# Performance work log

Measured on AMD Instinct MI355X. Metric: run time of the kernel, lower is better.

Reference implementation:

```python
import jax, jax.numpy as jnp
import numpy as np

D = 768
H = 8
HD = D // H
MLP = 3072
EPS = 1e-5


def _ln(x, g, b):
    mu = jnp.mean(x, axis=-1, keepdims=True)
    var = jnp.var(x, axis=-1, keepdims=True)
    return (x - mu) * jax.lax.rsqrt(var + EPS) * g + b


def setup_inputs() -> dict:
    key = jax.random.key(0)
    ks = jax.random.split(key, 20)
    B, N = 4, 2048
    s = 0.02
    inp = {
        "x": jax.random.normal(ks[0], (B, N, D), jnp.float32),
        "position_bias": jax.random.normal(ks[1], (N, N), jnp.float32),
        "wq": jax.random.normal(ks[2], (D, D), jnp.float32) * s,
        "bq": jnp.zeros((D,), jnp.float32),
        "wk": jax.random.normal(ks[3], (D, D), jnp.float32) * s,
        "bk": jnp.zeros((D,), jnp.float32),
        "wv": jax.random.normal(ks[4], (D, D), jnp.float32) * s,
        "bv": jnp.zeros((D,), jnp.float32),
        "wo": jax.random.normal(ks[5], (D, D), jnp.float32) * s,
        "bo": jnp.zeros((D,), jnp.float32),
        "g1": jnp.ones((D,), jnp.float32),
        "b1": jnp.zeros((D,), jnp.float32),
        "g2": jnp.ones((D,), jnp.float32),
        "b2": jnp.zeros((D,), jnp.float32),
        "w_ff1": jax.random.normal(ks[6], (D, MLP), jnp.float32) * s,
        "b_ff1": jnp.zeros((MLP,), jnp.float32),
        "w_ff2": jax.random.normal(ks[7], (MLP, D), jnp.float32) * s,
        "b_ff2": jnp.zeros((D,), jnp.float32),
    }
    return inp


def reference(x, position_bias, wq, bq, wk, bk, wv, bv, wo, bo, g1, b1, g2, b2, w_ff1, b_ff1, w_ff2, b_ff2):
    B, N, _ = x.shape
    scale = HD ** -0.5
    # pre-norm attention
    n1 = _ln(x, g1, b1)
    q = (n1 @ wq + bq).reshape(B, N, H, HD).transpose(0, 2, 1, 3)
    k = (n1 @ wk + bk).reshape(B, N, H, HD).transpose(0, 2, 1, 3)
    v = (n1 @ wv + bv).reshape(B, N, H, HD).transpose(0, 2, 1, 3)
    attn = jnp.einsum('bhqd,bhkd->bhqk', q, k) * scale  # [B,H,N,N]
    attn = attn + position_bias[None, None, :, :]
    attn = jax.nn.softmax(attn, axis=-1)
    out = jnp.einsum('bhqk,bhkd->bhqd', attn, v)
    out = out.transpose(0, 2, 1, 3).reshape(B, N, D)
    out = out @ wo + bo
    x = x + out
    # pre-norm GELU MLP (exact erf gelu, torch default)
    n2 = _ln(x, g2, b2)
    h = jax.nn.gelu(n2 @ w_ff1 + b_ff1, approximate=False)
    x = x + (h @ w_ff2 + b_ff2)
    return x
```

## Files before the change

kernel.cpp:

```cpp
#include <hip/hip_runtime.h>
#include <hip/hip_bf16.h>

#define D 768
#define H 8
#define HD 96
#define MLP 3072
#define NB 2048
#define BATCH 4

typedef __attribute__((ext_vector_type(8))) short short8;
typedef __attribute__((ext_vector_type(4))) short short4v;
typedef __attribute__((ext_vector_type(4))) float f32x4;
typedef __attribute__((ext_vector_type(16))) float f32x16;
typedef __attribute__((ext_vector_type(4))) int int4v;

typedef const __attribute__((address_space(1))) unsigned int gu32;
typedef __attribute__((address_space(3))) unsigned int lu32;

__device__ inline void gload16(const void* g, void* l){
  __builtin_amdgcn_global_load_lds((gu32*)g, (lu32*)l, 16, 0, 0);
}

__device__ inline short f2b(float f){
  __hip_bfloat16 h = __float2bfloat16(f);
  return *reinterpret_cast<short*>(&h);
}
__device__ inline float b2f(short s){
  return __uint_as_float(((unsigned)(unsigned short)s) << 16);
}
__device__ inline float fexp2(float x){ return __builtin_amdgcn_exp2f(x); }

__device__ inline unsigned cvtpk(float lo, float hi){
  unsigned r;
  asm volatile("v_cvt_pk_bf16_f32 %0, %1, %2" : "=v"(r) : "v"(lo), "v"(hi));
  return r;
}

__global__ __launch_bounds__(256) void mega_prep(
    const float* __restrict__ x, const float* __restrict__ g1, const float* __restrict__ b1,
    short* __restrict__ n1,
    const float* __restrict__ wq, const float* __restrict__ wk, const float* __restrict__ wv,
    const float* __restrict__ wo, const float* __restrict__ wf1, const float* __restrict__ wf2,
    const float* __restrict__ bq, const float* __restrict__ bk, const float* __restrict__ bv,
    short* __restrict__ wqkv_t, short* __restrict__ wo_t,
    short* __restrict__ w1_t, short* __restrict__ w2_t, float* __restrict__ bqkv,
    const float* __restrict__ pb, short* __restrict__ pbT)
{
  __shared__ float shbuf[32*33];
  int bx = blockIdx.x;
  int t = threadIdx.x;
  if (bx < 8192){
    int row = bx;
    const float* xr = x + (size_t)row*D;
    float v0=xr[t], v1=xr[t+256], v2=xr[t+512];
    float s=v0+v1+v2, ss=v0*v0+v1*v1+v2*v2;
    #pragma unroll
    for (int m=1;m<64;m<<=1){ s += __shfl_xor(s,m); ss += __shfl_xor(ss,m); }
    int w=t>>6, lane=t&63;
    if (!lane){ shbuf[w]=s; shbuf[4+w]=ss; }
    __syncthreads();
    s = shbuf[0]+shbuf[1]+shbuf[2]+shbuf[3];
    ss = shbuf[4]+shbuf[5]+shbuf[6]+shbuf[7];
    float mu = s*(1.f/768.f);
    float inv = rsqrtf(ss*(1.f/768.f) - mu*mu + 1e-5f);
    short* o = n1 + (size_t)row*D;
    o[t]     = f2b((v0-mu)*inv*g1[t]     + b1[t]);
    o[t+256] = f2b((v1-mu)*inv*g1[t+256] + b1[t+256]);
    o[t+512] = f2b((v2-mu)*inv*g1[t+512] + b1[t+512]);
  } else if (bx < 15104){
    int i = bx - 8192;
    if (i < 3){
      int j = i*256 + t;
      bqkv[j] = bq[j]; bqkv[768+j] = bk[j]; bqkv[1536+j] = bv[j];
    }
    const float* in; short* out; int K, Nc, bk_, bn_;
    if (i < 2304){
      int which = i/576, ii = i - which*576;
      bk_ = ii%24; bn_ = ii/24; K = 768; Nc = 768;
      if      (which==0){ in = wq; out = wqkv_t; }
      else if (which==1){ in = wk; out = wqkv_t + 768*768; }
      else if (which==2){ in = wv; out = wqkv_t + 2*768*768; }
      else              { in = wo; out = wo_t; }
    } else if (i < 4608){
      int ii = i - 2304; bk_ = ii%24; bn_ = ii/24; K = 768; Nc = 3072; in = wf1; out = w1_t;
    } else {
      int ii = i - 4608; bk_ = ii%96; bn_ = ii/96; K = 3072; Nc = 768; in = wf2; out = w2_t;
    }
    float (*tile)[33] = (float(*)[33])shbuf;
    int tx = t & 31, ty = t >> 5;
    #pragma unroll
    for (int j=0;j<4;++j)
      tile[ty + j*8][tx] = in[(size_t)(bk_*32 + ty + j*8)*Nc + bn_*32 + tx];
    __syncthreads();
    #pragma unroll
    for (int j=0;j<4;++j)
      out[(size_t)(bn_*32 + ty + j*8)*K + bk_*32 + tx] = f2b(tile[tx][ty + j*8]);
  } else {
    int i = bx - 15104;
    int qt = i & 63, kb = i >> 6;
    int l = t >> 2;
    int vbase = (t & 3) * 8;
    int q = qt*32 + (l & 31);
    int hi = l >> 5;
    const float L2E = 1.4426950408889634f;
    short8 o;
    #pragma unroll
    for (int j=0;j<8;++j){
      int v = vbase + j;
      int r = v & 15, tile_ = v >> 4;
      int k = kb*64 + tile_*32 + 8*(r>>2) + (r&3) + 4*hi;
      o[j] = f2b(pb[(size_t)q*NB + k] * L2E);
    }
    *(short8*)&pbT[(((size_t)(qt*32 + kb))*64 + l)*32 + vbase] = o;
  }
}

__global__ __launch_bounds__(256) void ln_k(const float* __restrict__ X, const float* __restrict__ gg,
                                            const float* __restrict__ bb, short* __restrict__ out){
  int row = blockIdx.x, t = threadIdx.x;
  const float* x = X + (size_t)row*D;
  float v0=x[t], v1=x[t+256], v2=x[t+512];
  float s=v0+v1+v2, ss=v0*v0+v1*v1+v2*v2;
  #pragma unroll
  for (int m=1;m<64;m<<=1){ s += __shfl_xor(s,m); ss += __shfl_xor(ss,m); }
  __shared__ float red[8];
  int w=t>>6, lane=t&63;
  if (!lane){ red[w]=s; red[4+w]=ss; }
  __syncthreads();
  s = red[0]+red[1]+red[2]+red[3];
  ss = red[4]+red[5]+red[6]+red[7];
  float mu = s*(1.f/768.f);
  float inv = rsqrtf(ss*(1.f/768.f) - mu*mu + 1e-5f);
  short* o = out + (size_t)row*D;
  o[t]     = f2b((v0-mu)*inv*gg[t]     + bb[t]);
  o[t+256] = f2b((v1-mu)*inv*gg[t+256] + bb[t+256]);
  o[t+512] = f2b((v2-mu)*inv*gg[t+512] + bb[t+512]);
}

template<int MODE>
__device__ __forceinline__ void gbt_body(char* AsB, char* BsB, int m0, int n0,
    const short* __restrict__ A, const short* __restrict__ Bt,
    const float* __restrict__ bias, void* __restrict__ Cout, int Nc, int K)
{
  int t = threadIdx.x;
  int lane = t & 63, w = t >> 6;
  int wm = w >> 1, wn = w & 1;
  int r = lane & 15, g = lane >> 4;
  const short* aSrc = A  + (size_t)(m0 + (t>>2))*K + (t&3)*8;
  const short* bSrc = Bt + (size_t)(n0 + (t>>2))*K + (t&3)*8;
  size_t rowK64 = (size_t)64*K;
  int dstOff = w*1024;
  f32x4 acc[4][4] = {};
  int nst = K >> 5;
  auto stage = [&](int u, int buf){
    char* ab = AsB + buf*8192;
    char* bb = BsB + buf*8192;
    int kt = u*32;
    gload16(aSrc + kt,          ab + dstOff);
    gload16(aSrc + kt + rowK64, ab + 4096 + dstOff);
    gload16(bSrc + kt,          bb + dstOff);
    gload16(bSrc + kt + rowK64, bb + 4096 + dstOff);
  };
  stage(0,0); stage(1,1);
  int cur = 0;
  for (int it=0; it<nst; ++it){
    if (it < nst-1) asm volatile("s_waitcnt vmcnt(4)" ::: "memory");
    else            asm volatile("s_waitcnt vmcnt(0)" ::: "memory");
    __builtin_amdgcn_s_barrier();
    __builtin_amdgcn_sched_barrier(0);
    if (it+2 < nst){
      int sb = cur+2; if (sb>=3) sb-=3;
      stage(it+2, sb);
    }
    short8 af[4], bfr[4];
    #pragma unroll
    for (int i=0;i<4;++i){
      af[i]  = *(const short8*)(AsB + cur*8192 + (wm*64 + i*16 + r)*64 + g*16);
      bfr[i] = *(const short8*)(BsB + cur*8192 + (wn*64 + i*16 + r)*64 + g*16);
    }
    #pragma unroll
    for (int i=0;i<4;++i)
      #pragma unroll
      for (int j=0;j<4;++j)
        acc[i][j] = __builtin_amdgcn_mfma_f32_16x16x32_bf16(af[i], bfr[j], acc[i][j], 0,0,0);
    cur = cur+1; if (cur>=3) cur-=3;
  }
  #pragma unroll
  for (int i=0;i<4;++i){
    #pragma unroll
    for (int j=0;j<4;++j){
      int col = n0 + wn*64 + j*16 + r;
      float bv = bias[col];
      #pragma unroll
      for (int q=0;q<4;++q){
        int row = m0 + wm*64 + i*16 + g*4 + q;
        size_t idx = (size_t)row*Nc + col;
        float val = acc[i][j][q] + bv;
        if constexpr (MODE==0){
          ((short*)Cout)[idx] = f2b(val);
        } else if constexpr (MODE==2){
          float ge = 0.5f*val*(1.f + erff(val*0.70710678118654752f));
          ((short*)Cout)[idx] = f2b(ge);
        }
      }
    }
  }
}

template<int MODE>
__device__ __forceinline__ void g64_body(char* AsB, char* BsB, int m0, int n0,
    const short* __restrict__ A, const short* __restrict__ Bt,
    const float* __restrict__ bias, const float* __restrict__ resid,
    void* __restrict__ Cout, int Nc, int K)
{
  int t = threadIdx.x;
  int lane = t & 63, w = t >> 6;
  int r = lane & 15, g = lane >> 4;
  const short* aSrc = A  + (size_t)(m0 + (t>>2))*K + (t&3)*8;
  const short* bSrc = Bt + (size_t)(n0 + (t>>2))*K + (t&3)*8;
  size_t rowK64 = (size_t)64*K;
  int dstOff = w*1024;
  f32x4 acc[4][2] = {};
  int nst = K >> 5;
  auto stage = [&](int u, int buf){
    char* ab = AsB + buf*4096;
    char* bb = BsB + buf*8192;
    int kt = u*32;
    gload16(aSrc + kt,          ab + dstOff);
    gload16(bSrc + kt,          bb + dstOff);
    gload16(bSrc + kt + rowK64, bb + 4096 + dstOff);
  };
  stage(0,0); stage(1,1);
  int cur = 0;
  for (int it=0; it<nst; ++it){
    if (it < nst-1) asm volatile("s_waitcnt vmcnt(3)" ::: "memory");
    else            asm volatile("s_waitcnt vmcnt(0)" ::: "memory");
    __builtin_amdgcn_s_barrier();
    __builtin_amdgcn_sched_barrier(0);
    if (it+2 < nst){
      int sb = cur+2; if (sb>=3) sb-=3;
      stage(it+2, sb);
    }
    short8 af[4], bfr[2];
    #pragma unroll
    for (int i=0;i<4;++i) af[i] = *(const short8*)(AsB + cur*4096 + (i*16 + r)*64 + g*16);
    #pragma unroll
    for (int j=0;j<2;++j) bfr[j] = *(const short8*)(BsB + cur*8192 + (w*32 + j*16 + r)*64 + g*16);
    #pragma unroll
    for (int i=0;i<4;++i)
      #pragma unroll
      for (int j=0;j<2;++j)
        acc[i][j] = __builtin_amdgcn_mfma_f32_16x16x32_bf16(af[i], bfr[j], acc[i][j], 0,0,0);
    cur = cur+1; if (cur>=3) cur-=3;
  }
  #pragma unroll
  for (int i=0;i<4;++i){
    #pragma unroll
    for (int j=0;j<2;++j){
      int col = n0 + w*32 + j*16 + r;
      #pragma unroll
      for (int q=0;q<4;++q){
        int row = m0 + i*16 + g*4 + q;
        if constexpr (MODE==1){
          size_t idx = (size_t)row*Nc + col;
          ((float*)Cout)[idx] = acc[i][j][q] + bias[col] + resid[idx];
        } else {
          int hh = row / 96, hd = row - hh*96;
          int bb = col >> 11, nn = col & 2047;
          size_t idx = ((size_t)((bb*8 + hh)*96 + hd))*2048 + nn;
          ((short*)Cout)[idx] = f2b(acc[i][j][q] + bias[row]);
        }
      }
    }
  }
}

template<int MODE>
__global__ __launch_bounds__(256) void gemm_bt(
    const short* __restrict__ A, const short* __restrict__ Bt,
    const float* __restrict__ bias, const float* __restrict__ resid,
    void* __restrict__ Cout, int Nc, int K)
{
  __shared__ __align__(16) char smem[49152];
  gbt_body<MODE>(smem, smem+24576, blockIdx.x*128, blockIdx.y*128, A, Bt, bias, Cout, Nc, K);
}

template<int MODE>
__global__ __launch_bounds__(256) void gemm64(
    const short* __restrict__ A, const short* __restrict__ Bt,
    const float* __restrict__ bias, const float* __restrict__ resid,
    void* __restrict__ Cout, int Nc, int K)
{
  __shared__ __align__(16) char smem[36864];
  g64_body<MODE>(smem, smem+12288, blockIdx.x*64, blockIdx.y*128, A, Bt, bias, resid, Cout, Nc, K);
}

__global__ __launch_bounds__(256) void qkv_fused(
    const short* __restrict__ n1, const short* __restrict__ wqkv_t, const float* __restrict__ bqkv,
    const short* __restrict__ wv_t, const float* __restrict__ bv,
    short* __restrict__ qkv, short* __restrict__ v_t)
{
  __shared__ __align__(16) char smem[49152];
  int bx = blockIdx.x;
  if (bx < 768){
    gbt_body<0>(smem, smem+24576, (bx&63)*128, (bx>>6)*128, n1, wqkv_t, bqkv, qkv, 1536, 768);
  } else {
    int i = bx - 768;
    g64_body<5>(smem, smem+12288, (i%12)*64, (i/12)*128, wv_t, n1, bv, nullptr, v_t, 0, 768);
  }
}

__global__ __launch_bounds__(512, 1) void attn_k(const short* __restrict__ qkv, const short* __restrict__ v_t,
                                                 const short* __restrict__ pbT, short* __restrict__ aout){
  int bx = blockIdx.x;
  int h = bx & 7, b = (bx>>3)&3, qb = bx>>5;
  int t = threadIdx.x, l = t & 63, w = t >> 6;
  int l31 = l & 31, hi = l >> 5, l7 = l & 7;
  __shared__ __align__(16) short Ks[2][64][128];
  __shared__ __align__(16) short Vs[2][96][64];
  const float SCALE2 = 0.10206207261596575f * 1.4426950408889634f;

  int qRow = qb*256 + w*32 + l31;
  const short* qg = qkv + (size_t)(b*NB + qRow)*1536 + h*HD;
  short8 qa[6];
  #pragma unroll
  for (int ds=0; ds<6; ++ds)
    qa[ds] = *(const short8*)&qg[ds*16 + hi*8];

  f32x16 oacc[3] = {};
  float m_run = -3.0e38f, l_run = 0.f;

  int r0 = t/12,        c0 = t%12;
  int s1 = 512 + t;
  int r1 = s1/12,       c1 = s1%12;
  int ldsK0 = r0*128 + (c0 ^ (r0&7))*8;
  int ldsK1 = r1*128 + (c1 ^ (r1&7))*8;
  const short* kgB = qkv + (size_t)(b*NB)*1536 + 768 + h*HD;
  bool wlow = (t < 256);
  int vr0 = t>>3,  vc0 = t&7;
  int vr1 = (512+t)>>3, vc1 = (512+t)&7;
  const short* vgB = v_t + (size_t)((b*H+h)*HD)*NB;
  const short* vsrc0 = vgB + (size_t)vr0*NB + (vc0 ^ (vr0&7))*8;
  const short* vsrc1 = vgB + (size_t)vr1*NB + (vc1 ^ (vr1&7))*8;
  const short* pbB = pbT + (((size_t)((qb*8 + w)*32))*64 + l)*32;

  {
    short8 ka = *(const short8*)&kgB[(size_t)r0*1536 + c0*8];
    short* ks0 = &Ks[0][0][0];
    *(short8*)(ks0 + ldsK0) = ka;
    if (wlow){
      short8 kb = *(const short8*)&kgB[(size_t)r1*1536 + c1*8];
      *(short8*)(ks0 + ldsK1) = kb;
    }
    gload16(vsrc0, (char*)Vs + w*1024);
    if (wlow) gload16(vsrc1, (char*)Vs + 8192 + w*1024);
  }
  __syncthreads();

  for (int kt=0; kt<32; ++kt){
    int cur = kt & 1;
    int kbase = kt*64;
    int kb2 = (kt < 31) ? (kbase + 64) : kbase;
    short8 kra = *(const short8*)&kgB[(size_t)(kb2 + r0)*1536 + c0*8];
    short8 krb = {};
    if (wlow) krb = *(const short8*)&kgB[(size_t)(kb2 + r1)*1536 + c1*8];
    const short* pbk = pbB + kt*2048;
    short8 pbr0 = *(const short8*)&pbk[0];
    short8 pbr1 = *(const short8*)&pbk[8];
    short8 pbr2 = *(const short8*)&pbk[16];
    short8 pbr3 = *(const short8*)&pbk[24];
    if (kt < 31){
      char* vbd = (char*)Vs + (cur^1)*12288;
      gload16(vsrc0 + kbase + 64, vbd + w*1024);
      if (wlow) gload16(vsrc1 + kbase + 64, vbd + 8192 + w*1024);
    }

    f32x16 sacc[2] = {};
    __builtin_amdgcn_s_setprio(1);
    #pragma unroll
    for (int tt=0; tt<2; ++tt){
      #pragma unroll
      for (int ds=0; ds<6; ++ds){
        short8 kf = *(const short8*)&Ks[cur][tt*32 + l31][((ds*2 + hi) ^ l7)*8];
        sacc[tt] = __builtin_amdgcn_mfma_f32_32x32x16_bf16(kf, qa[ds], sacc[tt], 0,0,0);
      }
    }
    __builtin_amdgcn_s_setprio(0);

    float vals[2][16];
    #pragma unroll
    for (int tt=0; tt<2; ++tt)
      #pragma unroll
      for (int r=0; r<16; ++r){
        int v = tt*16 + r;
        short pv = (v<8)?pbr0[v]:(v<16)?pbr1[v-8]:(v<24)?pbr2[v-16]:pbr3[v-24];
        vals[tt][r] = fmaf(sacc[tt][r], SCALE2, b2f(pv));
      }
    float pm = vals[0][0];
    #pragma unroll
    for (int tt=0; tt<2; ++tt)
      #pragma unroll
      for (int r=0; r<16; ++r) pm = fmaxf(pm, vals[tt][r]);
    pm = fmaxf(pm, __shfl_xor(pm, 32));
    if (__any(pm - m_run > 8.f)){
      float mn = fmaxf(m_run, pm);
      float f = fexp2(m_run - mn);
      l_run *= f; m_run = mn;
      int fi = __float_as_int(f);
      #pragma unroll
      for (int reg=0; reg<16; ++reg){
        int q = (reg&3) + 8*(reg>>2) + 4*hi;
        float fr = __int_as_float(__builtin_amdgcn_ds_bpermute(q<<2, fi));
        oacc[0][reg] *= fr; oacc[1][reg] *= fr; oacc[2][reg] *= fr;
      }
    }
    float p[2][16];
    float rs = 0.f;
    #pragma unroll
    for (int tt=0; tt<2; ++tt)
      #pragma unroll
      for (int r=0; r<16; ++r){
        p[tt][r] = fexp2(vals[tt][r] - m_run);
        rs += p[tt][r];
      }
    rs += __shfl_xor(rs, 32);
    l_run += rs;

    short8 pa[4];
    #pragma unroll
    for (int ks=0; ks<4; ++ks){
      int tt = ks>>1;
      int rb = (ks&1)*8;
      unsigned G0a = cvtpk(p[tt][rb+0], p[tt][rb+1]);
      unsigned G0b = cvtpk(p[tt][rb+2], p[tt][rb+3]);
      unsigned G1a = cvtpk(p[tt][rb+4], p[tt][rb+5]);
      unsigned G1b = cvtpk(p[tt][rb+6], p[tt][rb+7]);
      unsigned sG0a = (unsigned)__shfl_xor((int)G0a, 32);
      unsigned sG0b = (unsigned)__shfl_xor((int)G0b, 32);
      unsigned sG1a = (unsigned)__shfl_xor((int)G1a, 32);
      unsigned sG1b = (unsigned)__shfl_xor((int)G1b, 32);
      int4v wv;
      wv[0] = hi ? (int)sG1a : (int)G0a;
      wv[1] = hi ? (int)sG1b : (int)G0b;
      wv[2] = hi ? (int)G1a  : (int)sG0a;
      wv[3] = hi ? (int)G1b  : (int)sG0b;
      pa[ks] = __builtin_bit_cast(short8, wv);
    }

    __builtin_amdgcn_s_setprio(1);
    #pragma unroll
    for (int dt=0; dt<3; ++dt){
      #pragma unroll
      for (int ks=0; ks<4; ++ks){
        short8 vb = *(const short8*)&Vs[cur][dt*32 + l31][((ks*2 + hi) ^ l7)*8];
        oacc[dt] = __builtin_amdgcn_mfma_f32_32x32x16_bf16(pa[ks], vb, oacc[dt], 0,0,0);
      }
    }
    __builtin_amdgcn_s_setprio(0);

    if (kt < 31){
      short* ksn = &Ks[cur^1][0][0];
      *(short8*)(ksn + ldsK0) = kra;
      if (wlow) *(short8*)(ksn + ldsK1) = krb;
      __syncthreads();
    }
  }

  float inv_self = 1.f / l_run;
  int ii = __float_as_int(inv_self);
  #pragma unroll
  for (int reg=0; reg<16; ++reg){
    int q = (reg&3) + 8*(reg>>2) + 4*hi;
    float invq = __int_as_float(__builtin_amdgcn_ds_bpermute(q<<2, ii));
    int rowg = b*NB + qb*256 + w*32 + q;
    #pragma unroll
    for (int dt=0; dt<3; ++dt){
      int col = h*HD + dt*32 + l31;
      aout[(size_t)rowg*D + col] = f2b(oacc[dt][reg] * invq);
    }
  }
}

extern "C" void kernel_launch(void* const* d_in, const int* in_sizes, int n_in,
                              void* d_out, int out_size, void* d_ws, size_t ws_size,
                              hipStream_t stream){
  const float* x   = (const float*)d_in[0];
  const float* pb  = (const float*)d_in[1];
  const float* wq  = (const float*)d_in[2];
  const float* bq  = (const float*)d_in[3];
  const float* wk  = (const float*)d_in[4];
  const float* bk  = (const float*)d_in[5];
  const float* wv  = (const float*)d_in[6];
  const float* bv  = (const float*)d_in[7];
  const float* wo  = (const float*)d_in[8];
  const float* bo  = (const float*)d_in[9];
  const float* g1  = (const float*)d_in[10];
  const float* b1  = (const float*)d_in[11];
  const float* g2  = (const float*)d_in[12];
  const float* b2  = (const float*)d_in[13];
  const float* wf1 = (const float*)d_in[14];
  const float* bf1 = (const float*)d_in[15];
  const float* wf2 = (const float*)d_in[16];
  const float* bf2 = (const float*)d_in[17];
  float* out = (float*)d_out;

  char* p = (char*)d_ws;
  auto alloc = [&](size_t bytes){ char* q = p; p += (bytes + 255) & ~(size_t)255; return q; };
  short* wqkv_t = (short*)alloc((size_t)2304*768*2);
  short* wo_t   = (short*)alloc((size_t)768*768*2);
  short* w1_t   = (short*)alloc((size_t)3072*768*2);
  short* w2_t   = (short*)alloc((size_t)768*3072*2);
  float* bqkv   = (float*)alloc(2304*4);
  short* pbT    = (short*)alloc((size_t)2048*2048*2);
  float* x1     = (float*)alloc((size_t)8192*768*4);
  short* n2     = (short*)alloc((size_t)8192*768*2);
  short* n1     = (short*)alloc((size_t)8192*768*2);
  short* qkv    = (short*)alloc((size_t)8192*1536*2);
  short* v_t    = (short*)alloc((size_t)32*96*2048*2);
  short* hbuf   = n1;
  short* attn_o = n1;
  short* wv_t   = wqkv_t + (size_t)2*768*768;

  mega_prep<<<17152,256,0,stream>>>(x, g1, b1, n1,
                                    wq, wk, wv, wo, wf1, wf2, bq, bk, bv,
                                    wqkv_t, wo_t, w1_t, w2_t, bqkv, pb, pbT);
  qkv_fused<<<1536,256,0,stream>>>(n1, wqkv_t, bqkv, wv_t, bv, qkv, v_t);
  attn_k<<<256,512,0,stream>>>(qkv, v_t, pbT, attn_o);
  gemm64<1><<<dim3(128,6),256,0,stream>>>(attn_o, wo_t, bo, x, x1, 768, 768);
  ln_k<<<8192,256,0,stream>>>(x1, g2, b2, n2);
  gemm_bt<2><<<dim3(64,24),256,0,stream>>>(n2, w1_t, bf1, nullptr, hbuf, 3072, 768);
  gemm64<1><<<dim3(128,6),256,0,stream>>>(hbuf, w2_t, bf2, x1, out, 768, 3072);
}
```

Baseline: 302.7 us.

## Split attention key range across two blocks and merge partials

Splits the key dimension of the attention kernel into two halves, launching 512 blocks instead of 256. Each block writes unnormalized partial outputs as bf16 plus its running max and sum, and a new merge kernel combines them with log-sum-exp rescaling. The aim is to fill more of the GPU's compute units, since 256 blocks at one block per CU underfill the device. In exchange it adds an extra kernel launch, extra global traffic for the partials, and bf16 rounding of the unnormalized partial outputs.

```diff
diff --git a/kernel.cpp b/kernel.cpp
--- a/kernel.cpp
+++ b/kernel.cpp
@@ -311,9 +311,11 @@
 }
 
 __global__ __launch_bounds__(512, 1) void attn_k(const short* __restrict__ qkv, const short* __restrict__ v_t,
-                                                 const short* __restrict__ pbT, short* __restrict__ aout){
+                                                 const short* __restrict__ pbT,
+                                                 short* __restrict__ opart, float* __restrict__ mlbuf){
   int bx = blockIdx.x;
-  int h = bx & 7, b = (bx>>3)&3, qb = bx>>5;
+  int h = bx & 7, b = (bx>>3)&3, qb = (bx>>5)&7, half = bx>>8;
+  int k0 = half*16, kend = k0 + 16;
   int t = threadIdx.x, l = t & 63, w = t >> 6;
   int l31 = l & 31, hi = l >> 5, l7 = l & 7;
   __shared__ __align__(16) short Ks[2][64][128];
@@ -345,31 +347,32 @@
   const short* pbB = pbT + (((size_t)((qb*8 + w)*32))*64 + l)*32;
 
   {
-    short8 ka = *(const short8*)&kgB[(size_t)r0*1536 + c0*8];
+    int k00 = k0*64;
+    short8 ka = *(const short8*)&kgB[(size_t)(k00 + r0)*1536 + c0*8];
     short* ks0 = &Ks[0][0][0];
     *(short8*)(ks0 + ldsK0) = ka;
     if (wlow){
-      short8 kb = *(const short8*)&kgB[(size_t)r1*1536 + c1*8];
+      short8 kb = *(const short8*)&kgB[(size_t)(k00 + r1)*1536 + c1*8];
       *(short8*)(ks0 + ldsK1) = kb;
     }
-    gload16(vsrc0, (char*)Vs + w*1024);
-    if (wlow) gload16(vsrc1, (char*)Vs + 8192 + w*1024);
+    gload16(vsrc0 + k00, (char*)Vs + w*1024);
+    if (wlow) gload16(vsrc1 + k00, (char*)Vs + 8192 + w*1024);
   }
   __syncthreads();
 
-  for (int kt=0; kt<32; ++kt){
+  for (int kt=k0; kt<kend; ++kt){
     int cur = kt & 1;
     int kbase = kt*64;
-    int kb2 = (kt < 31) ? (kbase + 64) : kbase;
+    int kb2 = (kt < kend-1) ? (kbase + 64) : kbase;
     short8 kra = *(const short8*)&kgB[(size_t)(kb2 + r0)*1536 + c0*8];
     short8 krb = {};
     if (wlow) krb = *(const short8*)&kgB[(size_t)(kb2 + r1)*1536 + c1*8];
-    const short* pbk = pbB + kt*2048;
+    const short* pbk = pbB + (size_t)kt*2048;
     short8 pbr0 = *(const short8*)&pbk[0];
     short8 pbr1 = *(const short8*)&pbk[8];
     short8 pbr2 = *(const short8*)&pbk[16];
     short8 pbr3 = *(const short8*)&pbk[24];
-    if (kt < 31){
+    if (kt < kend-1){
       char* vbd = (char*)Vs + (cur^1)*12288;
       gload16(vsrc0 + kbase + 64, vbd + w*1024);
       if (wlow) gload16(vsrc1 + kbase + 64, vbd + 8192 + w*1024);
@@ -458,7 +461,7 @@
     }
     __builtin_amdgcn_s_setprio(0);
 
-    if (kt < 31){
+    if (kt < kend-1){
       short* ksn = &Ks[cur^1][0][0];
       *(short8*)(ksn + ldsK0) = kra;
       if (wlow) *(short8*)(ksn + ldsK1) = krb;
@@ -466,18 +469,46 @@
     }
   }
 
-  float inv_self = 1.f / l_run;
-  int ii = __float_as_int(inv_self);
+  if (hi == 0){
+    size_t mli = ((((size_t)half*4 + b)*8 + h)*2048 + qb*256 + w*32 + l31)*2;
+    mlbuf[mli]   = m_run;
+    mlbuf[mli+1] = l_run;
+  }
+  short* op = opart + (size_t)half*8192*768;
   #pragma unroll
   for (int reg=0; reg<16; ++reg){
     int q = (reg&3) + 8*(reg>>2) + 4*hi;
-    float invq = __int_as_float(__builtin_amdgcn_ds_bpermute(q<<2, ii));
     int rowg = b*NB + qb*256 + w*32 + q;
     #pragma unroll
     for (int dt=0; dt<3; ++dt){
       int col = h*HD + dt*32 + l31;
-      aout[(size_t)rowg*D + col] = f2b(oacc[dt][reg] * invq);
-    }
+      op[(size_t)rowg*D + col] = f2b(oacc[dt][reg]);
+    }
+  }
+}
+
+__global__ __launch_bounds__(256) void attn_merge(
+    const short* __restrict__ opart, const float* __restrict__ ml,
+    short* __restrict__ attn_o)
+{
+  int row = blockIdx.x;
+  int b = row >> 11, n = row & 2047;
+  int t = threadIdx.x;
+  const short* opA = opart;
+  const short* opB = opart + (size_t)8192*768;
+  #pragma unroll
+  for (int i=0;i<3;++i){
+    int c = t + i*256;
+    int h = c / 96;
+    size_t miA = ((((size_t)0*4 + b)*8 + h)*2048 + n)*2;
+    size_t miB = ((((size_t)1*4 + b)*8 + h)*2048 + n)*2;
+    float mA = ml[miA], lA = ml[miA+1];
+    float mB = ml[miB], lB = ml[miB+1];
+    float mF = fmaxf(mA, mB);
+    float fA = fexp2(mA - mF), fB = fexp2(mB - mF);
+    float linv = 1.f / (fA*lA + fB*lB);
+    size_t idx = (size_t)row*768 + c;
+    attn_o[idx] = f2b((fA*b2f(opA[idx]) + fB*b2f(opB[idx])) * linv);
   }
 }
 
@@ -513,19 +544,22 @@
   float* bqkv   = (float*)alloc(2304*4);
   short* pbT    = (short*)alloc((size_t)2048*2048*2);
   float* x1     = (float*)alloc((size_t)8192*768*4);
+  float* mlbuf  = (float*)alloc((size_t)2*4*8*2048*2*4);
   short* n2     = (short*)alloc((size_t)8192*768*2);
   short* n1     = (short*)alloc((size_t)8192*768*2);
   short* qkv    = (short*)alloc((size_t)8192*1536*2);
   short* v_t    = (short*)alloc((size_t)32*96*2048*2);
   short* hbuf   = n1;
   short* attn_o = n1;
+  short* opart  = (short*)x1;
   short* wv_t   = wqkv_t + (size_t)2*768*768;
 
   mega_prep<<<17152,256,0,stream>>>(x, g1, b1, n1,
                                     wq, wk, wv, wo, wf1, wf2, bq, bk, bv,
                                     wqkv_t, wo_t, w1_t, w2_t, bqkv, pb, pbT);
   qkv_fused<<<1536,256,0,stream>>>(n1, wqkv_t, bqkv, wv_t, bv, qkv, v_t);
-  attn_k<<<256,512,0,stream>>>(qkv, v_t, pbT, attn_o);
+  attn_k<<<512,512,0,stream>>>(qkv, v_t, pbT, opart, mlbuf);
+  attn_merge<<<8192,256,0,stream>>>(opart, mlbuf, attn_o);
   gemm64<1><<<dim3(128,6),256,0,stream>>>(attn_o, wo_t, bo, x, x1, 768, 768);
   ln_k<<<8192,256,0,stream>>>(x1, g2, b2, n2);
   gemm_bt<2><<<dim3(64,24),256,0,stream>>>(n2, w1_t, bf1, nullptr, hbuf, 3072, 768);
```

Result: slower. 319.8 us (+5.7%).
